# Kernel optimization log

Hardware: AMD Instinct MI355X
Metric: run time of the kernel (lower is better)

## Reference

```python
import jax, jax.numpy as jnp
import numpy as np

N_HEADS = 16
E = 1024
HEAD = E // N_HEADS

def setup_inputs() -> dict:
    key = jax.random.key(0)
    k1, k2, k3, k4 = jax.random.split(key, 4)
    x = jax.random.normal(k1, (4, 2048, E), dtype=jnp.float32)
    # Linear weights stored as (in, out) for x @ W
    W_kqv = jax.random.normal(k2, (E, 3 * E), dtype=jnp.float32) * (E ** -0.5)
    W_proj = jax.random.normal(k3, (E, E), dtype=jnp.float32) * (E ** -0.5)
    b_proj = jax.random.normal(k4, (E,), dtype=jnp.float32) * 0.02
    return {"x": x, "W_kqv": W_kqv, "W_proj": W_proj, "b_proj": b_proj}

def reference(x, W_kqv, W_proj, b_proj):
    B, T, Edim = x.shape
    kqv = x @ W_kqv  # [B,T,3E]
    k, q, v = jnp.split(kqv, 3, axis=-1)
    # [B,T,E] -> [B,H,T,D]
    def to_heads(t):
        return t.reshape(B, T, N_HEADS, HEAD).transpose(0, 2, 1, 3)
    k, q, v = to_heads(k), to_heads(q), to_heads(v)
    att = jnp.einsum('bhqd,bhkd->bhqk', q, k) * (HEAD ** -0.5)
    causal = jnp.tril(jnp.ones((T, T), dtype=bool))
    att = jnp.where(causal[None, None], att, jnp.float32(-jnp.inf))
    att = jax.nn.softmax(att, axis=-1)  # dropout p=0 (eval)
    x_att = jnp.einsum('bhqk,bhkd->bhqd', att, v)
    x_att = x_att.transpose(0, 2, 1, 3).reshape(B, T, Edim)
    return x_att @ W_proj + b_proj
```

## Files before the change

kernel.cpp:

```cpp
#include <hip/hip_runtime.h>
#include <hip/hip_bf16.h>


typedef __bf16 bf16_t;
typedef __bf16 bf16x8 __attribute__((ext_vector_type(8)));
typedef __bf16 bf16x4 __attribute__((ext_vector_type(4)));
typedef float  f32x4  __attribute__((ext_vector_type(4)));

#define GLD16(gp, lp) __builtin_amdgcn_global_load_lds(                        \
    (const __attribute__((address_space(1))) void*)(gp),                       \
    (__attribute__((address_space(3))) void*)(lp), 16, 0, 0)

static constexpr int kB = 4, kT = 2048, kE = 1024, kH = 16, kD = 64;
static constexpr int kM = kB * kT;
static constexpr int kN1 = 3 * kE;
static constexpr float kScale = 0.125f;
static constexpr float kShift = 10.0f;

__global__ void cvt_f32_bf16(const float* __restrict__ in,
                             bf16_t* __restrict__ out, int n4) {
  int i = blockIdx.x * 256 + threadIdx.x;
  if (i >= n4) return;
  float4 f = reinterpret_cast<const float4*>(in)[i];
  bf16x4 o = { (bf16_t)f.x, (bf16_t)f.y, (bf16_t)f.z, (bf16_t)f.w };
  reinterpret_cast<bf16x4*>(out)[i] = o;
}

__global__ void transpose_tile(const float* __restrict__ W,
                               bf16_t* __restrict__ Wt, int K, int N) {
  __shared__ bf16_t t[64][65];
  const int k0 = blockIdx.x * 64, n0 = blockIdx.y * 64;
  const int c = threadIdx.x & 63, r4 = threadIdx.x >> 6;
#pragma unroll
  for (int i = 0; i < 16; i++) {
    const int kk = r4 * 16 + i;
    t[kk][c] = (bf16_t)W[(size_t)(k0 + kk) * N + n0 + c];
  }
  __syncthreads();
#pragma unroll
  for (int i = 0; i < 16; i++) {
    const int nn = r4 * 16 + i;
    Wt[(size_t)(n0 + nn) * K + k0 + c] = t[c][nn];
  }
}

template <int MODE>
__global__ __launch_bounds__(256, 3)
void gemm_bt(const bf16_t* __restrict__ A, const bf16_t* __restrict__ Bt,
             float* __restrict__ Cout, const float* __restrict__ bias,
             bf16_t* __restrict__ Kh, bf16_t* __restrict__ Qh,
             bf16_t* __restrict__ Vt, int M, int N, int K) {
  constexpr int BM = 128, BN = 128, BK = 64;
  __shared__ __align__(16) bf16_t As[BM * BK];
  __shared__ __align__(16) bf16_t Bs[BN * BK];
  const int tid = threadIdx.x;
  const int lane = tid & 63, wave = tid >> 6;
  const int m0 = blockIdx.y * BM, n0 = blockIdx.x * BN;
  const int wr = (wave >> 1) * 64, wc = (wave & 1) * 64;
  const int l15 = lane & 15, l4 = lane >> 4;
  const int r8 = lane >> 3, c8 = lane & 7;

  f32x4 acc[4][4];
#pragma unroll
  for (int m = 0; m < 4; m++)
#pragma unroll
    for (int n = 0; n < 4; n++) acc[m][n] = f32x4{0.f, 0.f, 0.f, 0.f};

  for (int k0 = 0; k0 < K; k0 += BK) {
    const bf16_t* Ag = A + (size_t)(m0 + wave * 32) * K + k0;
    const bf16_t* Bg = Bt + (size_t)(n0 + wave * 32) * K + k0;
    bf16_t* Al = As + wave * 32 * BK;
    bf16_t* Bl = Bs + wave * 32 * BK;
#pragma unroll
    for (int i = 0; i < 4; i++) {
      GLD16(Ag + (size_t)(i * 8 + r8) * K + c8 * 8, Al + i * 8 * BK);
      GLD16(Bg + (size_t)(i * 8 + r8) * K + c8 * 8, Bl + i * 8 * BK);
    }
    __syncthreads();
#pragma unroll
    for (int ks = 0; ks < 2; ks++) {
      bf16x8 af[4], bfr[4];
#pragma unroll
      for (int m = 0; m < 4; m++)
        af[m] = *reinterpret_cast<const bf16x8*>(
            As + (wr + m * 16 + l15) * BK + ks * 32 + l4 * 8);
#pragma unroll
      for (int n = 0; n < 4; n++)
        bfr[n] = *reinterpret_cast<const bf16x8*>(
            Bs + (wc + n * 16 + l15) * BK + ks * 32 + l4 * 8);
#pragma unroll
      for (int m = 0; m < 4; m++)
#pragma unroll
        for (int n = 0; n < 4; n++)
          acc[m][n] = __builtin_amdgcn_mfma_f32_16x16x32_bf16(
              af[m], bfr[n], acc[m][n], 0, 0, 0);
    }
    __syncthreads();
  }

#pragma unroll
  for (int m = 0; m < 4; m++) {
#pragma unroll
    for (int n = 0; n < 4; n++) {
      const int gcol = n0 + wc + n * 16 + l15;
      const int growb = m0 + wr + m * 16 + l4 * 4;
      if constexpr (MODE == 0) {
        const int seg = gcol >> 10, idx = gcol & 1023;
        const int h = idx >> 6, d = idx & 63;
        const int b = growb >> 11, t = growb & 2047;
        if (seg == 2) {
          bf16x4 pv = { (bf16_t)acc[m][n][0], (bf16_t)acc[m][n][1],
                        (bf16_t)acc[m][n][2], (bf16_t)acc[m][n][3] };
          *reinterpret_cast<bf16x4*>(
              Vt + ((size_t)(b * 16 + h) * 64 + d) * 2048 + t) = pv;
        } else {
          bf16_t* tgt = (seg == 0) ? Kh : Qh;
          const float sc = (seg == 1) ? kScale : 1.0f;
#pragma unroll
          for (int j = 0; j < 4; j++)
            tgt[((size_t)(b * 16 + h) * 2048 + (t + j)) * 64 + d] =
                (bf16_t)(acc[m][n][j] * sc);
        }
      } else {
        const float bv = bias[gcol];
#pragma unroll
        for (int j = 0; j < 4; j++)
          Cout[(size_t)(growb + j) * N + gcol] = acc[m][n][j] + bv;
      }
    }
  }
}

__global__ __launch_bounds__(256, 3)
void attn_fwd(const bf16_t* __restrict__ Qh, const bf16_t* __restrict__ Kh,
              const bf16_t* __restrict__ Vt, bf16_t* __restrict__ xatt) {
  const int bx = blockIdx.x;
  const int qt = 15 - (bx >> 6);
  const int bh = bx & 63;
  const int b = bh >> 4, h = bh & 15;
  const bf16_t* Qp = Qh + (size_t)bh * kT * kD;
  const bf16_t* Kp = Kh + (size_t)bh * kT * kD;
  const bf16_t* Vp = Vt + (size_t)bh * kD * kT;
  __shared__ __align__(16) bf16_t Ks[2][64 * 64];
  __shared__ __align__(16) bf16_t Vs[2][64 * 64];
  __shared__ __align__(16) bf16_t Ps[128 * 64];
  const int tid = threadIdx.x, lane = tid & 63, wave = tid >> 6;
  const int l15 = lane & 15, l4 = lane >> 4;
  const int r8 = lane >> 3, c8 = lane & 7;
  const int qr = wave * 32;
  const int swc = (c8 ^ r8) * 8;
  const int swr = (l15 & 7) * 8;
  const int q0 = qt * 128;
  const int nkt = qt * 2 + 2;

  auto stage = [&](int buf, int kt) {
    const int k0 = kt * 64;
#pragma unroll
    for (int i = 0; i < 2; i++) {
      const int row = wave * 16 + i * 8 + r8;
      GLD16(Kp + (size_t)(k0 + row) * kD + swc,
            Ks[buf] + (wave * 16 + i * 8) * 64);
      GLD16(Vp + (size_t)row * kT + k0 + swc,
            Vs[buf] + (wave * 16 + i * 8) * 64);
    }
  };

  bf16x8 qf[2][2];
#pragma unroll
  for (int m = 0; m < 2; m++)
#pragma unroll
    for (int ks = 0; ks < 2; ks++)
      qf[m][ks] = *reinterpret_cast<const bf16x8*>(
          Qp + (size_t)(q0 + qr + m * 16 + l15) * kD + ks * 32 + l4 * 8);

  bf16x8 ones;
#pragma unroll
  for (int e = 0; e < 8; e++) ones[e] = (bf16_t)1.0f;

  f32x4 oacc[2][4];
  f32x4 lacc[2];
#pragma unroll
  for (int m = 0; m < 2; m++) {
    lacc[m] = f32x4{0.f, 0.f, 0.f, 0.f};
#pragma unroll
    for (int dn = 0; dn < 4; dn++) oacc[m][dn] = f32x4{0.f, 0.f, 0.f, 0.f};
  }

  stage(0, 0);
  __syncthreads();
  int cur = 0;
  for (int kt = 0; kt < nkt; kt++) {
    const int k0 = kt * 64;
    if (kt + 1 < nkt) stage(cur ^ 1, kt + 1);

    const bool active = (k0 <= q0 + qr + 31);
    if (active) {
      f32x4 s[2][4];
#pragma unroll
      for (int m = 0; m < 2; m++)
#pragma unroll
        for (int n = 0; n < 4; n++) s[m][n] = f32x4{0.f, 0.f, 0.f, 0.f};
      __builtin_amdgcn_s_setprio(1);
#pragma unroll
      for (int ks = 0; ks < 2; ks++) {
        bf16x8 kf[4];
#pragma unroll
        for (int n = 0; n < 4; n++)
          kf[n] = *reinterpret_cast<const bf16x8*>(
              Ks[cur] + (n * 16 + l15) * 64 + (((ks * 4 + l4) * 8) ^ swr));
#pragma unroll
        for (int m = 0; m < 2; m++)
#pragma unroll
          for (int n = 0; n < 4; n++)
            s[m][n] = __builtin_amdgcn_mfma_f32_16x16x32_bf16(
                qf[m][ks], kf[n], s[m][n], 0, 0, 0);
      }
      __builtin_amdgcn_s_setprio(0);

      if (k0 + 63 > q0 + qr) {
#pragma unroll
        for (int m = 0; m < 2; m++)
#pragma unroll
          for (int n = 0; n < 4; n++)
#pragma unroll
            for (int j = 0; j < 4; j++) {
              const int qg = q0 + qr + m * 16 + l4 * 4 + j;
              const int kg = k0 + n * 16 + l15;
              if (kg > qg) s[m][n][j] = -__builtin_inff();
            }
      }

#pragma unroll
      for (int m = 0; m < 2; m++)
#pragma unroll
        for (int n = 0; n < 4; n++)
#pragma unroll
          for (int j = 0; j < 4; j++) {
            const int pr = qr + m * 16 + l4 * 4 + j;
            Ps[pr * 64 + ((n * 16 + l15) ^ ((pr & 7) << 3))] =
                (bf16_t)__expf(s[m][n][j] - kShift);
          }

      __builtin_amdgcn_s_setprio(1);
#pragma unroll
      for (int ks = 0; ks < 2; ks++) {
        bf16x8 pf[2], vf[4];
#pragma unroll
        for (int m = 0; m < 2; m++)
          pf[m] = *reinterpret_cast<const bf16x8*>(
              Ps + (qr + m * 16 + l15) * 64 + (((ks * 4 + l4) * 8) ^ swr));
#pragma unroll
        for (int dn = 0; dn < 4; dn++)
          vf[dn] = *reinterpret_cast<const bf16x8*>(
              Vs[cur] + (dn * 16 + l15) * 64 + (((ks * 4 + l4) * 8) ^ swr));
#pragma unroll
        for (int m = 0; m < 2; m++) {
#pragma unroll
          for (int dn = 0; dn < 4; dn++)
            oacc[m][dn] = __builtin_amdgcn_mfma_f32_16x16x32_bf16(
                pf[m], vf[dn], oacc[m][dn], 0, 0, 0);
          lacc[m] = __builtin_amdgcn_mfma_f32_16x16x32_bf16(
              pf[m], ones, lacc[m], 0, 0, 0);
        }
      }
      __builtin_amdgcn_s_setprio(0);
    }
    __syncthreads();
    cur ^= 1;
  }

#pragma unroll
  for (int m = 0; m < 2; m++) {
    float inv[4];
#pragma unroll
    for (int j = 0; j < 4; j++) inv[j] = 1.f / lacc[m][j];
#pragma unroll
    for (int dn = 0; dn < 4; dn++)
#pragma unroll
      for (int j = 0; j < 4; j++) {
        const int t = q0 + qr + m * 16 + l4 * 4 + j;
        const int col = h * 64 + dn * 16 + l15;
        xatt[((size_t)b * kT + t) * kE + col] =
            (bf16_t)(oacc[m][dn][j] * inv[j]);
      }
  }
}

extern "C" void kernel_launch(void* const* d_in, const int* in_sizes, int n_in,
                              void* d_out, int out_size, void* d_ws,
                              size_t ws_size, hipStream_t stream) {
  const float* x     = (const float*)d_in[0];
  const float* Wkqv  = (const float*)d_in[1];
  const float* Wproj = (const float*)d_in[2];
  const float* bproj = (const float*)d_in[3];
  float* out = (float*)d_out;

  char* ws = (char*)d_ws;
  bf16_t* xb     = (bf16_t*)(ws);
  bf16_t* WkqvT  = (bf16_t*)(ws + 16777216);
  bf16_t* WprojT = (bf16_t*)(ws + 23068672);
  bf16_t* Qh     = (bf16_t*)(ws + 25165824);
  bf16_t* Kh     = (bf16_t*)(ws + 41943040);
  bf16_t* Vt     = (bf16_t*)(ws + 58720256);
  bf16_t* xatt   = (bf16_t*)(ws + 75497472);

  cvt_f32_bf16<<<(kM * kE / 4 + 255) / 256, 256, 0, stream>>>(x, xb, kM * kE / 4);
  transpose_tile<<<dim3(kE / 64, kN1 / 64), 256, 0, stream>>>(Wkqv, WkqvT, kE, kN1);
  transpose_tile<<<dim3(kE / 64, kE / 64), 256, 0, stream>>>(Wproj, WprojT, kE, kE);

  gemm_bt<0><<<dim3(kN1 / 128, kM / 128), 256, 0, stream>>>(
      xb, WkqvT, nullptr, nullptr, Kh, Qh, Vt, kM, kN1, kE);

  attn_fwd<<<dim3(16 * 64), 256, 0, stream>>>(Qh, Kh, Vt, xatt);

  gemm_bt<1><<<dim3(kE / 128, kM / 128), 256, 0, stream>>>(
      xatt, WprojT, out, bproj, nullptr, nullptr, nullptr, kM, kE, kE);
}
```

Baseline: 171.5 us.

## Triple-buffer GEMM K-loop with async global-to-LDS prefetch and fragment-ordered LDS

Replaces the single-buffered BK=64 GEMM main loop with a three-stage ring of BK=32 LDS buffers. Tiles are prefetched two steps ahead via global_load_lds, with explicit vmcnt waits and one barrier per iteration, so loads overlap with MFMA work. LDS is filled in MFMA fragment order so each lane reads a contiguous 16 bytes, and s_setprio is raised around the MFMA block. This gives more loop iterations and barriers, and the hand-written waitcnt logic is fragile. LDS use rises slightly, to 48 KB per block.

```diff
diff --git a/kernel.cpp b/kernel.cpp
--- a/kernel.cpp
+++ b/kernel.cpp
@@ -10,6 +10,8 @@
 #define GLD16(gp, lp) __builtin_amdgcn_global_load_lds(                        \
     (const __attribute__((address_space(1))) void*)(gp),                       \
     (__attribute__((address_space(3))) void*)(lp), 16, 0, 0)
+
+#define WAITV(n) asm volatile("s_waitcnt vmcnt(" #n ")" ::: "memory")
 
 static constexpr int kB = 4, kT = 2048, kE = 1024, kH = 16, kD = 64;
 static constexpr int kM = kB * kT;
@@ -46,19 +48,32 @@
 
 template <int MODE>
 __global__ __launch_bounds__(256, 3)
-void gemm_bt(const bf16_t* __restrict__ A, const bf16_t* __restrict__ Bt,
+void gemm_p3(const bf16_t* __restrict__ A, const bf16_t* __restrict__ Bt,
              float* __restrict__ Cout, const float* __restrict__ bias,
              bf16_t* __restrict__ Kh, bf16_t* __restrict__ Qh,
              bf16_t* __restrict__ Vt, int M, int N, int K) {
-  constexpr int BM = 128, BN = 128, BK = 64;
-  __shared__ __align__(16) bf16_t As[BM * BK];
-  __shared__ __align__(16) bf16_t Bs[BN * BK];
+  constexpr int BK = 32;
+  __shared__ __align__(16) bf16_t As_[3][128 * BK];
+  __shared__ __align__(16) bf16_t Bs_[3][128 * BK];
   const int tid = threadIdx.x;
   const int lane = tid & 63, wave = tid >> 6;
-  const int m0 = blockIdx.y * BM, n0 = blockIdx.x * BN;
+  const int m0 = blockIdx.y * 128, n0 = blockIdx.x * 128;
   const int wr = (wave >> 1) * 64, wc = (wave & 1) * 64;
   const int l15 = lane & 15, l4 = lane >> 4;
-  const int r8 = lane >> 3, c8 = lane & 7;
+  const int NT = K >> 5;
+  const bf16_t* Ag = A + (size_t)m0 * K;
+  const bf16_t* Bg = Bt + (size_t)n0 * K;
+
+  auto stage = [&](int kt, int bi) {
+    const int k0 = kt << 5;
+#pragma unroll
+    for (int i = 0; i < 2; i++) {
+      const size_t roff = (size_t)((i * 4 + wave) * 16 + l15) * K + k0 + l4 * 8;
+      const int dst = (i * 256 + wave * 64) * 8;
+      GLD16(Ag + roff, As_[bi] + dst);
+      GLD16(Bg + roff, Bs_[bi] + dst);
+    }
+  };
 
   f32x4 acc[4][4];
 #pragma unroll
@@ -66,36 +81,40 @@
 #pragma unroll
     for (int n = 0; n < 4; n++) acc[m][n] = f32x4{0.f, 0.f, 0.f, 0.f};
 
-  for (int k0 = 0; k0 < K; k0 += BK) {
-    const bf16_t* Ag = A + (size_t)(m0 + wave * 32) * K + k0;
-    const bf16_t* Bg = Bt + (size_t)(n0 + wave * 32) * K + k0;
-    bf16_t* Al = As + wave * 32 * BK;
-    bf16_t* Bl = Bs + wave * 32 * BK;
-#pragma unroll
-    for (int i = 0; i < 4; i++) {
-      GLD16(Ag + (size_t)(i * 8 + r8) * K + c8 * 8, Al + i * 8 * BK);
-      GLD16(Bg + (size_t)(i * 8 + r8) * K + c8 * 8, Bl + i * 8 * BK);
-    }
-    __syncthreads();
-#pragma unroll
-    for (int ks = 0; ks < 2; ks++) {
-      bf16x8 af[4], bfr[4];
-#pragma unroll
-      for (int m = 0; m < 4; m++)
-        af[m] = *reinterpret_cast<const bf16x8*>(
-            As + (wr + m * 16 + l15) * BK + ks * 32 + l4 * 8);
-#pragma unroll
-      for (int n = 0; n < 4; n++)
-        bfr[n] = *reinterpret_cast<const bf16x8*>(
-            Bs + (wc + n * 16 + l15) * BK + ks * 32 + l4 * 8);
-#pragma unroll
-      for (int m = 0; m < 4; m++)
-#pragma unroll
-        for (int n = 0; n < 4; n++)
-          acc[m][n] = __builtin_amdgcn_mfma_f32_16x16x32_bf16(
-              af[m], bfr[n], acc[m][n], 0, 0, 0);
-    }
-    __syncthreads();
+  const int wr4 = (wave >> 1) * 4, wc4 = (wave & 1) * 4;
+
+  stage(0, 0);
+  stage(1, 1);
+  WAITV(4);
+  __builtin_amdgcn_s_barrier();
+
+  int b0 = 0, b1 = 1, b2 = 2;
+#pragma unroll 1
+  for (int kt = 0; kt < NT; kt++) {
+    if (kt + 2 < NT) stage(kt + 2, b2);
+
+    bf16x8 af[4], bfr[4];
+#pragma unroll
+    for (int mf = 0; mf < 4; mf++)
+      af[mf] = *reinterpret_cast<const bf16x8*>(
+          As_[b0] + ((wr4 + mf) * 64 + lane) * 8);
+#pragma unroll
+    for (int nf = 0; nf < 4; nf++)
+      bfr[nf] = *reinterpret_cast<const bf16x8*>(
+          Bs_[b0] + ((wc4 + nf) * 64 + lane) * 8);
+    __builtin_amdgcn_s_setprio(1);
+#pragma unroll
+    for (int mf = 0; mf < 4; mf++)
+#pragma unroll
+      for (int nf = 0; nf < 4; nf++)
+        acc[mf][nf] = __builtin_amdgcn_mfma_f32_16x16x32_bf16(
+            af[mf], bfr[nf], acc[mf][nf], 0, 0, 0);
+    __builtin_amdgcn_s_setprio(0);
+
+    if (kt + 2 < NT) { WAITV(4); }
+    else if (kt + 1 < NT) { WAITV(0); }
+    __builtin_amdgcn_s_barrier();
+    const int tmp = b0; b0 = b1; b1 = b2; b2 = tmp;
   }
 
 #pragma unroll
@@ -308,11 +327,11 @@
   transpose_tile<<<dim3(kE / 64, kN1 / 64), 256, 0, stream>>>(Wkqv, WkqvT, kE, kN1);
   transpose_tile<<<dim3(kE / 64, kE / 64), 256, 0, stream>>>(Wproj, WprojT, kE, kE);
 
-  gemm_bt<0><<<dim3(kN1 / 128, kM / 128), 256, 0, stream>>>(
+  gemm_p3<0><<<dim3(kN1 / 128, kM / 128), 256, 0, stream>>>(
       xb, WkqvT, nullptr, nullptr, Kh, Qh, Vt, kM, kN1, kE);
 
   attn_fwd<<<dim3(16 * 64), 256, 0, stream>>>(Qh, Kh, Vt, xatt);
 
-  gemm_bt<1><<<dim3(kE / 128, kM / 128), 256, 0, stream>>>(
+  gemm_p3<1><<<dim3(kE / 128, kM / 128), 256, 0, stream>>>(
       xatt, WprojT, out, bproj, nullptr, nullptr, nullptr, kM, kE, kE);
 }
```

Result: slower. 212.2 us (+23.8%).
